# Kernel tuning notes

Measured on AMD Instinct MI355X. Metric: run time of the kernel, lower is better.

The kernel has to match this reference:

```python
import jax, jax.numpy as jnp
import numpy as np

jax.config.update("jax_enable_x64", True)  # torch casts to double for matrix_exp

EPS_DIAG = 1e-6


def setup_inputs() -> dict:
    key = jax.random.key(0)
    B, D, NB, S = 32, 128, 8, 128
    ks = jax.random.split(key, 9)
    return {
        "z0r": jax.random.normal(ks[0], (B, D), jnp.float32),
        "z0i": jax.random.normal(ks[1], (B, D), jnp.float32),
        # uniform grid: dt = time_steps[0] = 0.01, diffs == dt (uniform branch)
        "time_steps": (jnp.arange(S, dtype=jnp.float32) + 1.0) * 0.01,
        "k_coeffs": jax.random.normal(ks[2], (B, NB), jnp.float32),
        "r_coeffs": jax.random.normal(ks[3], (B, NB), jnp.float32),
        "alpha": jax.random.normal(ks[4], (B, 1), jnp.float32),
        "beta": jax.random.normal(ks[5], (B, 1), jnp.float32),
        "K_bases": jax.random.normal(ks[6], (NB, D, D), jnp.float32) * 0.01,
        "R_bases": jax.random.normal(ks[7], (NB, D, D), jnp.float32) * 0.01,
    }


def _build_generator(k_coeffs, r_coeffs, alpha, beta, K_bases, R_bases):
    # A = alpha * skew(K_sum) + beta * -(R_sum^T @ R_sum), per batch element
    K_sum = jnp.einsum("bn,nij->bij", k_coeffs, K_bases)
    R_sum = jnp.einsum("bn,nij->bij", r_coeffs, R_bases)
    skew = K_sum - jnp.swapaxes(K_sum, -1, -2)
    neg_gram = -jnp.einsum("bji,bjk->bik", R_sum, R_sum)  # -(R^T @ R)
    return alpha[..., None] * skew + beta[..., None] * neg_gram  # (B, D, D)


def _propagators(A, time_steps, uniform):
    D = A.shape[-1]
    S = time_steps.shape[0]
    if uniform:
        dt = time_steps[0]
        A64 = A.astype(jnp.float64) * dt.astype(jnp.float64) + EPS_DIAG * jnp.eye(D, dtype=jnp.float64)
        M = jax.vmap(jax.scipy.linalg.expm)(A64).astype(jnp.complex64)  # (B, D, D)
        # cumulative matrix powers M, M^2, ..., M^S via O(log S) associative scan
        Ms = jnp.broadcast_to(M[:, None], (M.shape[0], S, D, D))
        props = jax.lax.associative_scan(jnp.matmul, Ms, axis=1)
    else:
        A_t = A[:, None].astype(jnp.float64) * time_steps.astype(jnp.float64)[None, :, None, None]
        props = jax.vmap(jax.vmap(jax.scipy.linalg.expm))(A_t).astype(jnp.complex64)
    return props  # (B, S, D, D)


def reference(z0r, z0i, time_steps, k_coeffs, r_coeffs, alpha, beta, K_bases, R_bases):
    ts = np.asarray(time_steps)
    uniform = ts.shape[0] <= 1 or np.allclose(ts[1:] - ts[:-1], ts[0], atol=1e-6)
    A = _build_generator(k_coeffs, r_coeffs, alpha, beta, K_bases, R_bases)
    props = _propagators(A, time_steps, uniform)
    z = (z0r + 1j * z0i).astype(jnp.complex64)  # (B, D)
    # z_evolved[b, s, o] = sum_i z[b, i] * props[b, s, o, i]
    return jnp.einsum("bi,bsoi->bso", z, props)
```

## Files before the change

### kernel.cpp

```cpp
#include <hip/hip_runtime.h>

#define BATCH   32
#define DIM     128
#define NBASES  8
#define SSTEPS  128
#define LDA     136

typedef __attribute__((ext_vector_type(8)))  short s8v;
typedef __attribute__((ext_vector_type(4)))  short s4v;
typedef __attribute__((ext_vector_type(4)))  float f4v;
typedef __attribute__((ext_vector_type(16))) float f16v;

__device__ __forceinline__ f4v mf(s8v a, s8v b, f4v c) {
    return __builtin_amdgcn_mfma_f32_16x16x32_bf16(a, b, c, 0, 0, 0);
}
__device__ __forceinline__ f16v mf32(s8v a, s8v b, f16v c) {
    return __builtin_amdgcn_mfma_f32_32x32x16_bf16(a, b, c, 0, 0, 0);
}
__device__ __forceinline__ s8v ld8(const short* p) {
    return *reinterpret_cast<const s8v*>(p);
}
__device__ __forceinline__ s4v ld4(const short* p) {
    return *reinterpret_cast<const s4v*>(p);
}
__device__ __forceinline__ void st4(short* p, s4v v) {
    *reinterpret_cast<s4v*>(p) = v;
}
__device__ __forceinline__ float upbf(short h) {
    return __uint_as_float(((unsigned)(unsigned short)h) << 16);
}
__device__ __forceinline__ void splitbf(float v, short& hi, short& lo) {
    const unsigned u = __float_as_uint(v);
    hi = (short)(u >> 16);
    const float fh = __uint_as_float(u & 0xffff0000u);
    lo = (short)(__float_as_uint(v - fh) >> 16);
}

__device__ __forceinline__ void write_out(float* __restrict__ outF, int b, int sidx,
                                          int o, int c, float val,
                                          int interleaved, int out_size)
{
    if (interleaved) {
        const int oi = ((b * SSTEPS + sidx) * DIM + o) * 2 + c;
        if (oi < out_size) outF[oi] = val;
    } else if (c == 0) {
        const int oi = (b * SSTEPS + sidx) * DIM + o;
        if (oi < out_size) outF[oi] = val;
    }
}

template<bool TRO, bool NMO>
__device__ __forceinline__ void mm32(const short* __restrict__ Ah,
                                     const short* __restrict__ Al,
                                     const short* __restrict__ Bh,
                                     const short* __restrict__ Bl,
                                     f16v& acc, f16v& acct,
                                     int mb, int nb, int lane)
{
    const int l31 = lane & 31, koc = (lane >> 5) * 8;
    #pragma unroll
    for (int ks = 0; ks < 8; ++ks) {
        const int ko = ks * 16 + koc;
        const s8v ah = ld8(Ah + (mb + l31) * LDA + ko);
        const s8v al = ld8(Al + (mb + l31) * LDA + ko);
        const s8v bh = ld8(Bh + (nb + l31) * LDA + ko);
        const s8v bl = ld8(Bl + (nb + l31) * LDA + ko);
        if (TRO) {
            acc = mf32(ah, bh, acc);
            acc = mf32(ah, bl, acc);
            acc = mf32(al, bh, acc);
        }
        if (NMO) {
            acct = mf32(bh, ah, acct);
            acct = mf32(bl, ah, acct);
            acct = mf32(bh, al, acct);
        }
    }
}

__global__ __launch_bounds__(256)
void sum_kr(const float* __restrict__ kco, const float* __restrict__ rco,
            const float* __restrict__ KB,  const float* __restrict__ RB,
            float* __restrict__ ws)
{
    const int b = blockIdx.x >> 3, s = blockIdx.x & 7, t = threadIdx.x;
    const int boff = s * 16 * DIM + t * 8;
    const int r = s * 16 + (t >> 4), c = (t & 15) * 8;
    float kc[NBASES], rc[NBASES];
    #pragma unroll
    for (int n = 0; n < NBASES; ++n) {
        kc[n] = kco[b * NBASES + n];
        rc[n] = rco[b * NBASES + n];
    }
    float4 ka = {0.f,0.f,0.f,0.f}, kb4 = {0.f,0.f,0.f,0.f};
    float4 ra = {0.f,0.f,0.f,0.f}, rb4 = {0.f,0.f,0.f,0.f};
    #pragma unroll
    for (int n = 0; n < NBASES; ++n) {
        const float4 k0 = *reinterpret_cast<const float4*>(KB + n * DIM * DIM + boff);
        const float4 k1 = *reinterpret_cast<const float4*>(KB + n * DIM * DIM + boff + 4);
        const float4 r0 = *reinterpret_cast<const float4*>(RB + n * DIM * DIM + boff);
        const float4 r1 = *reinterpret_cast<const float4*>(RB + n * DIM * DIM + boff + 4);
        ka.x += kc[n] * k0.x; ka.y += kc[n] * k0.y; ka.z += kc[n] * k0.z; ka.w += kc[n] * k0.w;
        kb4.x += kc[n] * k1.x; kb4.y += kc[n] * k1.y; kb4.z += kc[n] * k1.z; kb4.w += kc[n] * k1.w;
        ra.x += rc[n] * r0.x; ra.y += rc[n] * r0.y; ra.z += rc[n] * r0.z; ra.w += rc[n] * r0.w;
        rb4.x += rc[n] * r1.x; rb4.y += rc[n] * r1.y; rb4.z += rc[n] * r1.z; rb4.w += rc[n] * r1.w;
    }
    float* Ks  = ws + (size_t)b * DIM * DIM;
    float* KsT = ws + (size_t)BATCH * DIM * DIM + (size_t)b * DIM * DIM;
    float* RsT = ws + (size_t)2 * BATCH * DIM * DIM + (size_t)b * DIM * DIM;
    *reinterpret_cast<float4*>(Ks + boff)     = ka;
    *reinterpret_cast<float4*>(Ks + boff + 4) = kb4;
    const float kv[8] = {ka.x, ka.y, ka.z, ka.w, kb4.x, kb4.y, kb4.z, kb4.w};
    const float rv[8] = {ra.x, ra.y, ra.z, ra.w, rb4.x, rb4.y, rb4.z, rb4.w};
    #pragma unroll
    for (int j = 0; j < 8; ++j) {
        KsT[(c + j) * DIM + r] = kv[j];
        RsT[(c + j) * DIM + r] = rv[j];
    }
}

template<int PRE>
__global__ __launch_bounds__(1024) __attribute__((amdgpu_waves_per_eu(4, 4)))
void htg_mfma(const float* __restrict__ z0r, const float* __restrict__ z0i,
              const float* __restrict__ ts,  const float* __restrict__ kco,
              const float* __restrict__ rco, const float* __restrict__ alp,
              const float* __restrict__ bet, const float* __restrict__ KB,
              const float* __restrict__ RB,  const float* __restrict__ wsum,
              float* __restrict__ outF, int interleaved, int out_size)
{
    __shared__ short nm_hi[DIM * LDA], nm_lo[DIM * LDA];
    __shared__ short tr_hi[DIM * LDA], tr_lo[DIM * LDA];
    __shared__ short ht_hi[32 * LDA],  ht_lo[32 * LDA];

    const int b = blockIdx.x, t = threadIdx.x;
    const int w = t >> 6, lane = t & 63;
    const int l15 = lane & 15, quad = lane >> 4;
    const int l31 = lane & 31, kq = lane >> 5;
    const f4v z4 = {0.f, 0.f, 0.f, 0.f};
    const int mb = (w & 3) * 32, nb = (w >> 2) * 32;

    if (PRE) {
        const float* RsT = wsum + (size_t)2 * BATCH * DIM * DIM + (size_t)b * DIM * DIM;
        #pragma unroll
        for (int q = 0; q < 4; ++q) {
            const int e = q * 4096 + t * 4;
            const float4 rv = *reinterpret_cast<const float4*>(RsT + e);
            const int row = e >> 7, colr = e & 127;
            const float rr[4] = {rv.x, rv.y, rv.z, rv.w};
            s4v h4, l4;
            #pragma unroll
            for (int j = 0; j < 4; ++j) {
                short hi, lo; splitbf(rr[j], hi, lo);
                h4[j] = hi; l4[j] = lo;
            }
            st4(&tr_hi[row * LDA + colr], h4);
            st4(&tr_lo[row * LDA + colr], l4);
        }
        if (t < 2 * DIM) {
            const int c = t >> 7, o = t & 127;
            const float zv = (c == 0) ? z0r[b * DIM + o] : z0i[b * DIM + o];
            short hi, lo; splitbf(zv, hi, lo);
            ht_hi[c * LDA + o] = hi; ht_lo[c * LDA + o] = lo;
        }
    } else {
        float rc[NBASES], kc[NBASES];
        #pragma unroll
        for (int n = 0; n < NBASES; ++n) {
            rc[n] = rco[b * NBASES + n];
            kc[n] = kco[b * NBASES + n];
        }
        #pragma unroll
        for (int q = 0; q < 4; ++q) {
            const int e = q * 4096 + t * 4;
            float4 r4 = {0.f, 0.f, 0.f, 0.f}, k4 = {0.f, 0.f, 0.f, 0.f};
            #pragma unroll
            for (int n = 0; n < NBASES; ++n) {
                const float4 rvv = *reinterpret_cast<const float4*>(RB + n * DIM * DIM + e);
                const float4 kvv = *reinterpret_cast<const float4*>(KB + n * DIM * DIM + e);
                r4.x += rc[n] * rvv.x; r4.y += rc[n] * rvv.y;
                r4.z += rc[n] * rvv.z; r4.w += rc[n] * rvv.w;
                k4.x += kc[n] * kvv.x; k4.y += kc[n] * kvv.y;
                k4.z += kc[n] * kvv.z; k4.w += kc[n] * kvv.w;
            }
            const int r = e >> 7, c = e & 127;
            const float rr[4] = {r4.x, r4.y, r4.z, r4.w};
            const float kk[4] = {k4.x, k4.y, k4.z, k4.w};
            s4v kh, kl;
            #pragma unroll
            for (int j = 0; j < 4; ++j) {
                short hi, lo;
                splitbf(rr[j], hi, lo);
                tr_hi[(c + j) * LDA + r] = hi; tr_lo[(c + j) * LDA + r] = lo;
                splitbf(kk[j], hi, lo);
                kh[j] = hi; kl[j] = lo;
            }
            st4(&nm_hi[r * LDA + c], kh);
            st4(&nm_lo[r * LDA + c], kl);
        }
        if (t < 2 * DIM) {
            const int c = t >> 7, o = t & 127;
            const float zv = (c == 0) ? z0r[b * DIM + o] : z0i[b * DIM + o];
            short hi, lo; splitbf(zv, hi, lo);
            ht_hi[c * LDA + o] = hi; ht_lo[c * LDA + o] = lo;
        }
    }
    __syncthreads();

    f16v acc, acct;
    float xsave[16];
    float xsaveT[16];

    float kd[4][4], kdT[4][4];
    if (PRE) {
        const float* Ks  = wsum + (size_t)b * DIM * DIM;
        const float* KsT = wsum + (size_t)BATCH * DIM * DIM + (size_t)b * DIM * DIM;
        #pragma unroll
        for (int r4 = 0; r4 < 4; ++r4) {
            const int row0 = mb + 8 * r4 + 4 * kq;
            const int col  = nb + l31;
            const int rt0  = nb + 8 * r4 + 4 * kq;
            const int ct   = mb + l31;
            #pragma unroll
            for (int j = 0; j < 4; ++j) {
                kd[r4][j]  = Ks[(row0 + j) * DIM + col] - KsT[(row0 + j) * DIM + col];
                kdT[r4][j] = KsT[(rt0 + j) * DIM + ct]  - Ks[(rt0 + j) * DIM + ct];
            }
        }
    } else {
        #pragma unroll
        for (int r4 = 0; r4 < 4; ++r4) {
            {
                const int row0 = mb + 8 * r4 + 4 * kq;
                const int col  = nb + l31;
                const s4v k2h = ld4(&nm_hi[col * LDA + row0]);
                const s4v k2l = ld4(&nm_lo[col * LDA + row0]);
                #pragma unroll
                for (int j = 0; j < 4; ++j)
                    kd[r4][j] = (upbf(nm_hi[(row0 + j) * LDA + col]) +
                                 upbf(nm_lo[(row0 + j) * LDA + col]))
                              - (upbf(k2h[j]) + upbf(k2l[j]));
            }
            {
                const int rt0 = nb + 8 * r4 + 4 * kq;
                const int ct  = mb + l31;
                const s4v k1h = ld4(&nm_hi[ct * LDA + rt0]);
                const s4v k1l = ld4(&nm_lo[ct * LDA + rt0]);
                #pragma unroll
                for (int j = 0; j < 4; ++j)
                    kdT[r4][j] = (upbf(k1h[j]) + upbf(k1l[j]))
                               - (upbf(nm_hi[(rt0 + j) * LDA + ct]) +
                                  upbf(nm_lo[(rt0 + j) * LDA + ct]));
            }
        }
    }
    #pragma unroll
    for (int i = 0; i < 16; ++i) { acc[i] = 0.f; acct[i] = 0.f; }
    mm32<true, true>(tr_hi, tr_lo, tr_hi, tr_lo, acc, acct, mb, nb, lane);
    __syncthreads();
    {
        const float alpha = alp[b], beta = bet[b], dtf = ts[0];
        #pragma unroll
        for (int r4 = 0; r4 < 4; ++r4) {
            {
                const int row0 = mb + 8 * r4 + 4 * kq;
                const int col  = nb + l31;
                s4v h4, l4;
                #pragma unroll
                for (int j = 0; j < 4; ++j) {
                    float x = (alpha * kd[r4][j] - beta * acc[4 * r4 + j]) * dtf;
                    if (row0 + j == col) x += 1e-6f;
                    xsave[4 * r4 + j] = x;
                    short hi, lo; splitbf(x, hi, lo);
                    h4[j] = hi; l4[j] = lo;
                }
                st4(&tr_hi[col * LDA + row0], h4);
                st4(&tr_lo[col * LDA + row0], l4);
            }
            {
                const int rt0 = nb + 8 * r4 + 4 * kq;
                const int ct  = mb + l31;
                s4v h4, l4;
                #pragma unroll
                for (int j = 0; j < 4; ++j) {
                    float x = (alpha * kdT[r4][j] - beta * acct[4 * r4 + j]) * dtf;
                    if (ct == rt0 + j) x += 1e-6f;
                    xsaveT[4 * r4 + j] = x;
                    short hi, lo; splitbf(x, hi, lo);
                    h4[j] = hi; l4[j] = lo;
                }
                st4(&nm_hi[ct * LDA + rt0], h4);
                st4(&nm_lo[ct * LDA + rt0], l4);
            }
        }
    }
    __syncthreads();

    #pragma unroll
    for (int i = 0; i < 16; ++i) { acc[i] = 0.f; acct[i] = 0.f; }
    mm32<true, true>(nm_hi, nm_lo, tr_hi, tr_lo, acc, acct, mb, nb, lane);
    __syncthreads();
    #pragma unroll
    for (int r4 = 0; r4 < 4; ++r4) {
        {
            const int row0 = mb + 8 * r4 + 4 * kq;
            const int col  = nb + l31;
            s4v h4, l4;
            #pragma unroll
            for (int j = 0; j < 4; ++j) {
                const float xv = xsave[4 * r4 + j];
                const float cv = acc[4 * r4 + j];
                const float a2 = xv * (1.f / 6.f) + cv * (1.f / 24.f);
                xsave[4 * r4 + j] = ((row0 + j == col) ? 1.f : 0.f) + xv + 0.5f * cv;
                short hi, lo; splitbf(a2, hi, lo);
                h4[j] = hi; l4[j] = lo;
            }
            st4(&tr_hi[col * LDA + row0], h4);
            st4(&tr_lo[col * LDA + row0], l4);
        }
        {
            const int rt0 = nb + 8 * r4 + 4 * kq;
            const int ct  = mb + l31;
            s4v h4, l4;
            #pragma unroll
            for (int j = 0; j < 4; ++j) {
                const float xT = xsaveT[4 * r4 + j];
                const float cT = acct[4 * r4 + j];
                xsaveT[4 * r4 + j] = ((ct == rt0 + j) ? 1.f : 0.f) + xT + 0.5f * cT;
                short hi, lo; splitbf(cT, hi, lo);
                h4[j] = hi; l4[j] = lo;
            }
            st4(&nm_hi[ct * LDA + rt0], h4);
            st4(&nm_lo[ct * LDA + rt0], l4);
        }
    }
    __syncthreads();

    #pragma unroll
    for (int i = 0; i < 16; ++i) { acc[i] = xsave[i]; acct[i] = xsaveT[i]; }
    mm32<true, true>(nm_hi, nm_lo, tr_hi, tr_lo, acc, acct, mb, nb, lane);
    __syncthreads();
    #pragma unroll
    for (int r4 = 0; r4 < 4; ++r4) {
        {
            const int row0 = mb + 8 * r4 + 4 * kq;
            const int col  = nb + l31;
            s4v h4, l4;
            #pragma unroll
            for (int j = 0; j < 4; ++j) {
                short hi, lo; splitbf(acc[4 * r4 + j], hi, lo);
                h4[j] = hi; l4[j] = lo;
            }
            st4(&tr_hi[col * LDA + row0], h4);
            st4(&tr_lo[col * LDA + row0], l4);
        }
        {
            const int rt0 = nb + 8 * r4 + 4 * kq;
            const int ct  = mb + l31;
            s4v h4, l4;
            #pragma unroll
            for (int j = 0; j < 4; ++j) {
                short hi, lo; splitbf(acct[4 * r4 + j], hi, lo);
                h4[j] = hi; l4[j] = lo;
            }
            st4(&nm_hi[ct * LDA + rt0], h4);
            st4(&nm_lo[ct * LDA + rt0], l4);
        }
    }
    __syncthreads();

    #pragma unroll
    for (int stage = 0; stage < 3; ++stage) {
        const int J = 1 << stage;
        f4v ar = z4;
        #pragma unroll
        for (int i = 0; i < 16; ++i) { acc[i] = 0.f; acct[i] = 0.f; }
        if (w < 8) {
            #pragma unroll
            for (int kk = 0; kk < DIM; kk += 32) {
                const int ko = kk + quad * 8;
                const s8v rah = ld8(nm_hi + (w * 16 + l15) * LDA + ko);
                const s8v ral = ld8(nm_lo + (w * 16 + l15) * LDA + ko);
                const s8v rbh = ld8(ht_hi + l15 * LDA + ko);
                const s8v rbl = ld8(ht_lo + l15 * LDA + ko);
                ar = mf(rah, rbh, ar);
                ar = mf(rah, rbl, ar);
                ar = mf(ral, rbh, ar);
            }
        }
        mm32<true, true>(nm_hi, nm_lo, tr_hi, tr_lo, acc, acct, mb, nb, lane);
        __syncthreads();
        if (w < 8 && l15 < 2 * J) {
            const int o0 = w * 16 + quad * 4;
            const int sidx = (l15 >> 1) + J - 1;
            s4v h4, l4;
            #pragma unroll
            for (int r = 0; r < 4; ++r) {
                short hi, lo; splitbf(ar[r], hi, lo);
                h4[r] = hi; l4[r] = lo;
                write_out(outF, b, sidx, o0 + r, l15 & 1, ar[r], interleaved, out_size);
            }
            st4(&ht_hi[(l15 + 2 * J) * LDA + o0], h4);
            st4(&ht_lo[(l15 + 2 * J) * LDA + o0], l4);
        }
        #pragma unroll
        for (int r4 = 0; r4 < 4; ++r4) {
            {
                const int row0 = mb + 8 * r4 + 4 * kq;
                const int col  = nb + l31;
                s4v h4, l4;
                #pragma unroll
                for (int j = 0; j < 4; ++j) {
                    short hi, lo; splitbf(acc[4 * r4 + j], hi, lo);
                    h4[j] = hi; l4[j] = lo;
                }
                st4(&tr_hi[col * LDA + row0], h4);
                st4(&tr_lo[col * LDA + row0], l4);
            }
            {
                const int rt0 = nb + 8 * r4 + 4 * kq;
                const int ct  = mb + l31;
                s4v h4, l4;
                #pragma unroll
                for (int j = 0; j < 4; ++j) {
                    short hi, lo; splitbf(acct[4 * r4 + j], hi, lo);
                    h4[j] = hi; l4[j] = lo;
                }
                st4(&nm_hi[ct * LDA + rt0], h4);
                st4(&nm_lo[ct * LDA + rt0], l4);
            }
        }
        __syncthreads();
    }

    {
        const int J = 8;
        f4v ar = z4;
        #pragma unroll
        for (int i = 0; i < 16; ++i) acct[i] = 0.f;
        if (w < 8) {
            #pragma unroll
            for (int kk = 0; kk < DIM; kk += 32) {
                const int ko = kk + quad * 8;
                const s8v rah = ld8(nm_hi + (w * 16 + l15) * LDA + ko);
                const s8v ral = ld8(nm_lo + (w * 16 + l15) * LDA + ko);
                const s8v rbh = ld8(ht_hi + l15 * LDA + ko);
                const s8v rbl = ld8(ht_lo + l15 * LDA + ko);
                ar = mf(rah, rbh, ar);
                ar = mf(rah, rbl, ar);
                ar = mf(ral, rbh, ar);
            }
        }
        mm32<false, true>(nm_hi, nm_lo, tr_hi, tr_lo, acc, acct, mb, nb, lane);
        __syncthreads();
        if (w < 8 && l15 < 2 * J) {
            const int o0 = w * 16 + quad * 4;
            const int sidx = (l15 >> 1) + J - 1;
            s4v h4, l4;
            #pragma unroll
            for (int r = 0; r < 4; ++r) {
                short hi, lo; splitbf(ar[r], hi, lo);
                h4[r] = hi; l4[r] = lo;
                write_out(outF, b, sidx, o0 + r, l15 & 1, ar[r], interleaved, out_size);
            }
            st4(&ht_hi[(l15 + 2 * J) * LDA + o0], h4);
            st4(&ht_lo[(l15 + 2 * J) * LDA + o0], l4);
        }
        #pragma unroll
        for (int r4 = 0; r4 < 4; ++r4) {
            const int rt0 = nb + 8 * r4 + 4 * kq;
            const int ct  = mb + l31;
            s4v h4, l4;
            #pragma unroll
            for (int j = 0; j < 4; ++j) {
                short hi, lo; splitbf(acct[4 * r4 + j], hi, lo);
                h4[j] = hi; l4[j] = lo;
            }
            st4(&nm_hi[ct * LDA + rt0], h4);
            st4(&nm_lo[ct * LDA + rt0], l4);
        }
        __syncthreads();
    }

    const int sw = w >> 1, ct = w & 1;
    s8v vah[4], val[4];
    #pragma unroll
    for (int k4 = 0; k4 < 4; ++k4) {
        const int ko = k4 * 32 + quad * 8;
        vah[k4] = ld8(nm_hi + (sw * 16 + l15) * LDA + ko);
        val[k4] = ld8(nm_lo + (sw * 16 + l15) * LDA + ko);
    }
    short *rh_hi = ht_hi, *rh_lo = ht_lo;
    short *wh_hi = tr_hi, *wh_lo = tr_lo;
    #pragma unroll
    for (int q = 1; q <= 8; ++q) {
        f4v a2 = z4;
        #pragma unroll
        for (int k4 = 0; k4 < 4; ++k4) {
            const int ko = k4 * 32 + quad * 8;
            const s8v bh = ld8(rh_hi + (ct * 16 + l15) * LDA + ko);
            const s8v bl = ld8(rh_lo + (ct * 16 + l15) * LDA + ko);
            a2 = mf(vah[k4], bh, a2);
            a2 = mf(vah[k4], bl, a2);
            a2 = mf(val[k4], bh, a2);
        }
        {
            const int o0 = sw * 16 + quad * 4;
            const int n = ct * 16 + l15;
            const int sidx = 16 * q + (n >> 1) - 1;
            s4v h4, l4;
            #pragma unroll
            for (int r = 0; r < 4; ++r) {
                short hi, lo; splitbf(a2[r], hi, lo);
                h4[r] = hi; l4[r] = lo;
                if (sidx < SSTEPS)
                    write_out(outF, b, sidx, o0 + r, n & 1, a2[r], interleaved, out_size);
            }
            if (q < 8) {
                st4(&wh_hi[n * LDA + o0], h4);
                st4(&wh_lo[n * LDA + o0], l4);
            }
        }
        __syncthreads();
        short* tp;
        tp = rh_hi; rh_hi = wh_hi; wh_hi = tp;
        tp = rh_lo; rh_lo = wh_lo; wh_lo = tp;
    }
}

extern "C" void kernel_launch(void* const* d_in, const int* in_sizes, int n_in,
                              void* d_out, int out_size, void* d_ws, size_t ws_size,
                              hipStream_t stream)
{
    (void)in_sizes; (void)n_in;
    const float* z0r = (const float*)d_in[0];
    const float* z0i = (const float*)d_in[1];
    const float* ts  = (const float*)d_in[2];
    const float* kco = (const float*)d_in[3];
    const float* rco = (const float*)d_in[4];
    const float* alp = (const float*)d_in[5];
    const float* bet = (const float*)d_in[6];
    const float* KB  = (const float*)d_in[7];
    const float* RB  = (const float*)d_in[8];
    float* outF = (float*)d_out;

    const int interleaved = (out_size >= 2 * BATCH * SSTEPS * DIM) ? 1 : 0;
    const size_t ws_needed = (size_t)3 * BATCH * DIM * DIM * sizeof(float);

    if (d_ws != nullptr && ws_size >= ws_needed) {
        float* ws = (float*)d_ws;
        sum_kr<<<dim3(BATCH * 8), dim3(256), 0, stream>>>(kco, rco, KB, RB, ws);
        htg_mfma<1><<<dim3(BATCH), dim3(1024), 0, stream>>>(
            z0r, z0i, ts, kco, rco, alp, bet, KB, RB, ws, outF, interleaved, out_size);
    } else {
        htg_mfma<0><<<dim3(BATCH), dim3(1024), 0, stream>>>(
            z0r, z0i, ts, kco, rco, alp, bet, KB, RB, nullptr, outF, interleaved, out_size);
    }
}
```

Before: 114.9 us.

## Truncate Taylor expm by one matmul and defer output stores to kernel end

Drops the highest-order Taylor term in the matrix exponential. It builds I + X + C/2 directly instead of running one more 128x128 matmul and its split-to-bf16 store pass, which removes a matmul and two barriers. The power and scan outputs are now kept in registers (arsave, wout) and written to global memory in one batch after all matmul work, so global stores no longer sit between barrier phases. The last loop iteration also skips its barrier. The costs are a lower-order series approximation with some accuracy risk, and more live registers, which may hurt occupancy.

```diff
diff --git a/kernel.cpp b/kernel.cpp
--- a/kernel.cpp
+++ b/kernel.cpp
@@ -207,8 +207,7 @@
     __syncthreads();
 
     f16v acc, acct;
-    float xsave[16];
-    float xsaveT[16];
+    float xsave[16], xsaveT[16];
 
     float kd[4][4], kdT[4][4];
     if (PRE) {
@@ -307,11 +306,9 @@
             s4v h4, l4;
             #pragma unroll
             for (int j = 0; j < 4; ++j) {
-                const float xv = xsave[4 * r4 + j];
-                const float cv = acc[4 * r4 + j];
-                const float a2 = xv * (1.f / 6.f) + cv * (1.f / 24.f);
-                xsave[4 * r4 + j] = ((row0 + j == col) ? 1.f : 0.f) + xv + 0.5f * cv;
-                short hi, lo; splitbf(a2, hi, lo);
+                const float m = ((row0 + j == col) ? 1.f : 0.f)
+                              + xsave[4 * r4 + j] + 0.5f * acc[4 * r4 + j];
+                short hi, lo; splitbf(m, hi, lo);
                 h4[j] = hi; l4[j] = lo;
             }
             st4(&tr_hi[col * LDA + row0], h4);
@@ -323,10 +320,9 @@
             s4v h4, l4;
             #pragma unroll
             for (int j = 0; j < 4; ++j) {
-                const float xT = xsaveT[4 * r4 + j];
-                const float cT = acct[4 * r4 + j];
-                xsaveT[4 * r4 + j] = ((ct == rt0 + j) ? 1.f : 0.f) + xT + 0.5f * cT;
-                short hi, lo; splitbf(cT, hi, lo);
+                const float m = ((ct == rt0 + j) ? 1.f : 0.f)
+                              + xsaveT[4 * r4 + j] + 0.5f * acct[4 * r4 + j];
+                short hi, lo; splitbf(m, hi, lo);
                 h4[j] = hi; l4[j] = lo;
             }
             st4(&nm_hi[ct * LDA + rt0], h4);
@@ -335,38 +331,7 @@
     }
     __syncthreads();
 
-    #pragma unroll
-    for (int i = 0; i < 16; ++i) { acc[i] = xsave[i]; acct[i] = xsaveT[i]; }
-    mm32<true, true>(nm_hi, nm_lo, tr_hi, tr_lo, acc, acct, mb, nb, lane);
-    __syncthreads();
-    #pragma unroll
-    for (int r4 = 0; r4 < 4; ++r4) {
-        {
-            const int row0 = mb + 8 * r4 + 4 * kq;
-            const int col  = nb + l31;
-            s4v h4, l4;
-            #pragma unroll
-            for (int j = 0; j < 4; ++j) {
-                short hi, lo; splitbf(acc[4 * r4 + j], hi, lo);
-                h4[j] = hi; l4[j] = lo;
-            }
-            st4(&tr_hi[col * LDA + row0], h4);
-            st4(&tr_lo[col * LDA + row0], l4);
-        }
-        {
-            const int rt0 = nb + 8 * r4 + 4 * kq;
-            const int ct  = mb + l31;
-            s4v h4, l4;
-            #pragma unroll
-            for (int j = 0; j < 4; ++j) {
-                short hi, lo; splitbf(acct[4 * r4 + j], hi, lo);
-                h4[j] = hi; l4[j] = lo;
-            }
-            st4(&nm_hi[ct * LDA + rt0], h4);
-            st4(&nm_lo[ct * LDA + rt0], l4);
-        }
-    }
-    __syncthreads();
+    float arsave[4][4];
 
     #pragma unroll
     for (int stage = 0; stage < 3; ++stage) {
@@ -389,15 +354,15 @@
         }
         mm32<true, true>(nm_hi, nm_lo, tr_hi, tr_lo, acc, acct, mb, nb, lane);
         __syncthreads();
+        #pragma unroll
+        for (int r = 0; r < 4; ++r) arsave[stage][r] = ar[r];
         if (w < 8 && l15 < 2 * J) {
             const int o0 = w * 16 + quad * 4;
-            const int sidx = (l15 >> 1) + J - 1;
             s4v h4, l4;
             #pragma unroll
             for (int r = 0; r < 4; ++r) {
                 short hi, lo; splitbf(ar[r], hi, lo);
                 h4[r] = hi; l4[r] = lo;
-                write_out(outF, b, sidx, o0 + r, l15 & 1, ar[r], interleaved, out_size);
             }
             st4(&ht_hi[(l15 + 2 * J) * LDA + o0], h4);
             st4(&ht_lo[(l15 + 2 * J) * LDA + o0], l4);
@@ -452,15 +417,15 @@
         }
         mm32<false, true>(nm_hi, nm_lo, tr_hi, tr_lo, acc, acct, mb, nb, lane);
         __syncthreads();
+        #pragma unroll
+        for (int r = 0; r < 4; ++r) arsave[3][r] = ar[r];
         if (w < 8 && l15 < 2 * J) {
             const int o0 = w * 16 + quad * 4;
-            const int sidx = (l15 >> 1) + J - 1;
             s4v h4, l4;
             #pragma unroll
             for (int r = 0; r < 4; ++r) {
                 short hi, lo; splitbf(ar[r], hi, lo);
                 h4[r] = hi; l4[r] = lo;
-                write_out(outF, b, sidx, o0 + r, l15 & 1, ar[r], interleaved, out_size);
             }
             st4(&ht_hi[(l15 + 2 * J) * LDA + o0], h4);
             st4(&ht_lo[(l15 + 2 * J) * LDA + o0], l4);
@@ -489,6 +454,7 @@
         vah[k4] = ld8(nm_hi + (sw * 16 + l15) * LDA + ko);
         val[k4] = ld8(nm_lo + (sw * 16 + l15) * LDA + ko);
     }
+    float wout[8][4];
     short *rh_hi = ht_hi, *rh_lo = ht_lo;
     short *wh_hi = tr_hi, *wh_lo = tr_lo;
     #pragma unroll
@@ -503,27 +469,51 @@
             a2 = mf(vah[k4], bl, a2);
             a2 = mf(val[k4], bh, a2);
         }
-        {
+        #pragma unroll
+        for (int r = 0; r < 4; ++r) wout[q - 1][r] = a2[r];
+        if (q < 8) {
             const int o0 = sw * 16 + quad * 4;
             const int n = ct * 16 + l15;
-            const int sidx = 16 * q + (n >> 1) - 1;
             s4v h4, l4;
             #pragma unroll
             for (int r = 0; r < 4; ++r) {
                 short hi, lo; splitbf(a2[r], hi, lo);
                 h4[r] = hi; l4[r] = lo;
-                if (sidx < SSTEPS)
-                    write_out(outF, b, sidx, o0 + r, n & 1, a2[r], interleaved, out_size);
-            }
-            if (q < 8) {
-                st4(&wh_hi[n * LDA + o0], h4);
-                st4(&wh_lo[n * LDA + o0], l4);
-            }
-        }
-        __syncthreads();
+            }
+            st4(&wh_hi[n * LDA + o0], h4);
+            st4(&wh_lo[n * LDA + o0], l4);
+            __syncthreads();
+        }
         short* tp;
         tp = rh_hi; rh_hi = wh_hi; wh_hi = tp;
         tp = rh_lo; rh_lo = wh_lo; wh_lo = tp;
+    }
+
+    #pragma unroll
+    for (int stage = 0; stage < 4; ++stage) {
+        const int J = 1 << stage;
+        if (w < 8 && l15 < 2 * J) {
+            const int o0 = w * 16 + quad * 4;
+            const int sidx = (l15 >> 1) + J - 1;
+            #pragma unroll
+            for (int r = 0; r < 4; ++r)
+                write_out(outF, b, sidx, o0 + r, l15 & 1, arsave[stage][r],
+                          interleaved, out_size);
+        }
+    }
+    {
+        const int o0 = sw * 16 + quad * 4;
+        const int n = ct * 16 + l15;
+        #pragma unroll
+        for (int q = 1; q <= 8; ++q) {
+            const int sidx = 16 * q + (n >> 1) - 1;
+            if (sidx < SSTEPS) {
+                #pragma unroll
+                for (int r = 0; r < 4; ++r)
+                    write_out(outF, b, sidx, o0 + r, n & 1, wout[q - 1][r],
+                              interleaved, out_size);
+            }
+        }
     }
 }
 
```

Result: slower. 117.5 us (+2.2%).
